# Performance work log

Hardware: AMD Instinct MI355X
Metric: run time of the kernel (lower is better)

## Reference

```python
import jax, jax.numpy as jnp
import numpy as np

B, L, DM, H, PD = 2, 1024, 512, 8, 64
D = DM // H  # head_dim = 64
NEG = -10000.0


def setup_inputs() -> dict:
    key = jax.random.key(0)
    ks = jax.random.split(key, 12)
    s = 1.0 / np.sqrt(DM)
    sp = 1.0 / np.sqrt(PD)
    return {
        "x": jax.random.normal(ks[0], (B, L, DM), dtype=jnp.float32),
        "z": jax.random.normal(ks[1], (B, L, L, PD), dtype=jnp.float32),
        "residue_mask": jnp.ones((B, L), dtype=bool),
        "Wq": jax.random.normal(ks[2], (DM, DM), dtype=jnp.float32) * s,
        "bq": jnp.zeros((DM,), dtype=jnp.float32),
        "Wk": jax.random.normal(ks[3], (DM, DM), dtype=jnp.float32) * s,
        "bk": jnp.zeros((DM,), dtype=jnp.float32),
        "Wv": jax.random.normal(ks[4], (DM, DM), dtype=jnp.float32) * s,
        "bv": jnp.zeros((DM,), dtype=jnp.float32),
        "Wo": jax.random.normal(ks[5], (DM, DM), dtype=jnp.float32) * s,
        "bo": jnp.zeros((DM,), dtype=jnp.float32),
        "Wpb": jax.random.normal(ks[6], (PD, H), dtype=jnp.float32) * sp,
    }


def reference(x, z, residue_mask, Wq, bq, Wk, bk, Wv, bv, Wo, bo, Wpb):
    b, l, c = x.shape
    scale = 1.0 / np.sqrt(D)
    # projections -> (B, H, L, D)
    q = (x @ Wq + bq).reshape(b, l, H, D).transpose(0, 2, 1, 3)
    k = (x @ Wk + bk).reshape(b, l, H, D).transpose(0, 2, 1, 3)
    v = (x @ Wv + bv).reshape(b, l, H, D).transpose(0, 2, 1, 3)
    # pair bias: (B, L, L, PD) @ (PD, H) -> (B, H, L, L)
    bias = jnp.einsum('bijp,ph->bhij', z, Wpb)
    logits = jnp.einsum('bhid,bhjd->bhij', q, k) * scale + bias
    key_ok = residue_mask[:, None, None, :]
    query_ok = residue_mask[:, None, :, None]
    logits = jnp.where(key_ok, logits, NEG)
    logits = jnp.where(query_ok, logits, NEG)
    attn = jax.nn.softmax(logits, axis=-1)
    out = jnp.einsum('bhij,bhjd->bhid', attn, v)
    out = out.transpose(0, 2, 1, 3).reshape(b, l, c)
    return out @ Wo + bo
```

## Files before the change

### kernel.cpp

```cpp
#include <hip/hip_runtime.h>

typedef __bf16 bf16;
typedef __attribute__((ext_vector_type(4))) __bf16 bf16x4;
typedef __attribute__((ext_vector_type(8))) __bf16 bf16x8;
typedef __attribute__((ext_vector_type(4))) float f32x4;
typedef __attribute__((ext_vector_type(4))) _Float16 f16x4;
typedef __attribute__((ext_vector_type(2))) _Float16 f16x2;

#define B_   2
#define L_   1024
#define DM_  512
#define H_   8
#define D_   64
#define PD_  64
#define NEG_VAL -10000.0f

#define XB_N   (2048*512)
#define WT_N   (1536*512)
#define WTO_N  (512*512)
#define WTPB_N (16*64)

static __device__ __forceinline__ f32x4 mfma_bf16(bf16x8 a, bf16x8 b, f32x4 c) {
  return __builtin_amdgcn_mfma_f32_16x16x32_bf16(a, b, c, 0, 0, 0);
}

__global__ __launch_bounds__(256) void prep_kernel(
    const float* __restrict__ x, const float* __restrict__ Wq, const float* __restrict__ Wk,
    const float* __restrict__ Wv, const float* __restrict__ Wo, const float* __restrict__ Wpb,
    bf16* __restrict__ xb, bf16* __restrict__ Wt, bf16* __restrict__ Wto, bf16* __restrict__ Wtpb) {
  const int total = XB_N + WT_N + WTO_N + WTPB_N;
  for (int idx = blockIdx.x * 256 + threadIdx.x; idx < total; idx += gridDim.x * 256) {
    if (idx < XB_N) {
      xb[idx] = (bf16)x[idx];
    } else if (idx < XB_N + WT_N) {
      int t = idx - XB_N;
      int n = t >> 9, kk = t & 511;
      int sel = n >> 9, nn = n & 511;
      const float* W = sel == 0 ? Wq : (sel == 1 ? Wk : Wv);
      Wt[t] = (bf16)W[kk * 512 + nn];
    } else if (idx < XB_N + WT_N + WTO_N) {
      int t = idx - XB_N - WT_N;
      int n = t >> 9, kk = t & 511;
      Wto[t] = (bf16)Wo[kk * 512 + n];
    } else {
      int t = idx - XB_N - WT_N - WTO_N;
      int n = t >> 6, kk = t & 63;
      Wtpb[t] = (n < 8) ? (bf16)Wpb[kk * 8 + n] : (bf16)0.0f;
    }
  }
}

__global__ __launch_bounds__(256) void qkv_gemm(
    const bf16* __restrict__ xb, const bf16* __restrict__ Wt,
    const float* __restrict__ bq, const float* __restrict__ bk, const float* __restrict__ bv,
    bf16* __restrict__ qb, bf16* __restrict__ kb, bf16* __restrict__ vT) {
  int wid = blockIdx.x * 4 + (threadIdx.x >> 6);
  int lane = threadIdx.x & 63;
  int mt = wid / 48, nt = wid - mt * 48;
  int row0 = mt * 32, col0 = nt * 32;
  int lr = lane & 15, lg = lane >> 4;
  const bf16* a0p = xb + (row0 + lr) * 512 + lg * 8;
  const bf16* a1p = a0p + 16 * 512;
  const bf16* b0p = Wt + (col0 + lr) * 512 + lg * 8;
  const bf16* b1p = b0p + 16 * 512;
  f32x4 acc00 = {0.f,0.f,0.f,0.f}, acc01 = acc00, acc10 = acc00, acc11 = acc00;
#pragma unroll
  for (int kk = 0; kk < 512; kk += 32) {
    bf16x8 a0 = *reinterpret_cast<const bf16x8*>(a0p + kk);
    bf16x8 a1 = *reinterpret_cast<const bf16x8*>(a1p + kk);
    bf16x8 b0 = *reinterpret_cast<const bf16x8*>(b0p + kk);
    bf16x8 b1 = *reinterpret_cast<const bf16x8*>(b1p + kk);
    acc00 = mfma_bf16(a0, b0, acc00);
    acc01 = mfma_bf16(a0, b1, acc01);
    acc10 = mfma_bf16(a1, b0, acc10);
    acc11 = mfma_bf16(a1, b1, acc11);
  }
#pragma unroll
  for (int ni = 0; ni < 2; ++ni) {
    int col = col0 + ni * 16 + lr;
    int wsel = col >> 9;
    int ncol = col & 511;
    int h = ncol >> 6, d = ncol & 63;
    const float* bias = wsel == 0 ? bq : (wsel == 1 ? bk : bv);
    float bval = bias[ncol];
#pragma unroll
    for (int mi = 0; mi < 2; ++mi) {
      f32x4 acc = (mi == 0) ? (ni == 0 ? acc00 : acc01) : (ni == 0 ? acc10 : acc11);
      int m0 = row0 + mi * 16 + lg * 4;
      int bidx = m0 >> 10, l0 = m0 & 1023;
      if (wsel == 2) {
        bf16x4 pv;
#pragma unroll
        for (int r = 0; r < 4; ++r) pv[r] = (bf16)(acc[r] + bval);
        *reinterpret_cast<bf16x4*>(vT + ((long)(bidx * H_ + h) * D_ + d) * L_ + l0) = pv;
      } else if (wsel == 0) {
#pragma unroll
        for (int r = 0; r < 4; ++r)
          qb[((long)(bidx * H_ + h) * L_ + l0 + r) * D_ + d] = (bf16)((acc[r] + bval) * 0.125f);
      } else {
#pragma unroll
        for (int r = 0; r < 4; ++r)
          kb[((long)(bidx * H_ + h) * L_ + l0 + r) * D_ + d] = (bf16)(acc[r] + bval);
      }
    }
  }
}

__global__ __launch_bounds__(256) void bias_gemm(
    const float* __restrict__ z, const bf16* __restrict__ Wtpb, _Float16* __restrict__ biasbuf) {
  __shared__ _Float16 bt[8][72];
  int w = threadIdx.x >> 6, lane = threadIdx.x & 63;
  int lr = lane & 15, lg = lane >> 4;
  long p0 = (long)blockIdx.x * 64 + w * 16;
  const float* zr = z + (p0 + lr) * 64;
  f32x4 z0 = *reinterpret_cast<const f32x4*>(zr + lg * 8);
  f32x4 z1 = *reinterpret_cast<const f32x4*>(zr + lg * 8 + 4);
  f32x4 z2 = *reinterpret_cast<const f32x4*>(zr + 32 + lg * 8);
  f32x4 z3 = *reinterpret_cast<const f32x4*>(zr + 32 + lg * 8 + 4);
  bf16x8 a0, a1;
#pragma unroll
  for (int e = 0; e < 4; ++e) { a0[e] = (bf16)z0[e]; a0[e + 4] = (bf16)z1[e]; }
#pragma unroll
  for (int e = 0; e < 4; ++e) { a1[e] = (bf16)z2[e]; a1[e + 4] = (bf16)z3[e]; }
  bf16x8 b0 = *reinterpret_cast<const bf16x8*>(Wtpb + lr * 64 + lg * 8);
  bf16x8 b1 = *reinterpret_cast<const bf16x8*>(Wtpb + lr * 64 + 32 + lg * 8);
  f32x4 acc = {0.f, 0.f, 0.f, 0.f};
  acc = mfma_bf16(a0, b0, acc);
  acc = mfma_bf16(a1, b1, acc);
  if (lr < 8) {
    f16x4 hv;
#pragma unroll
    for (int r = 0; r < 4; ++r) hv[r] = (_Float16)acc[r];
    *reinterpret_cast<f16x4*>(&bt[lr][w * 16 + lg * 4]) = hv;
  }
  __syncthreads();
  {
    int h = threadIdx.x >> 5, part = threadIdx.x & 31;
    long pb = (long)blockIdx.x * 64;
    int b = (int)(pb >> 20), i = ((int)(pb >> 10)) & 1023, j0 = (int)pb & 1023;
    _Float16* dst = biasbuf + ((((long)b * H_ + h) * L_ + i) << 10) + j0 + part * 2;
    *reinterpret_cast<f16x2*>(dst) = *reinterpret_cast<const f16x2*>(&bt[h][part * 2]);
  }
}

__global__ __launch_bounds__(256) void attn_kernel(
    const bf16* __restrict__ qb, const bf16* __restrict__ kb, const bf16* __restrict__ vT,
    const _Float16* __restrict__ biasbuf, const int* __restrict__ mask, bf16* __restrict__ attn_out) {
  __shared__ bf16  p_lds[4][16][64];
  __shared__ float o_lds[4][16][64];
  __shared__ float m_lds[4][16];
  __shared__ float l_lds[4][16];
  int bid = blockIdx.x;
  int b = bid >> 9, h = (bid >> 6) & 7, it = bid & 63;
  int i0 = it * 16;
  int tid = threadIdx.x, w = tid >> 6, lane = tid & 63, lr = lane & 15, lg = lane >> 4;

  const bf16* qrow = qb + ((long)(b * H_ + h) * L_ + i0 + lr) * D_ + lg * 8;
  bf16x8 qa0 = *reinterpret_cast<const bf16x8*>(qrow);
  bf16x8 qa1 = *reinterpret_cast<const bf16x8*>(qrow + 32);
  const bf16* kbase = kb + (long)(b * H_ + h) * L_ * D_;
  const bf16* vbase = vT + (long)(b * H_ + h) * D_ * L_;
  const _Float16* bias_base = biasbuf + ((long)(b * H_ + h) * L_ + i0) * L_;
  const int* mrow_mask = mask + b * L_;

  bool qok[4];
#pragma unroll
  for (int r = 0; r < 4; ++r) qok[r] = mrow_mask[i0 + lg * 4 + r] != 0;

  float mr[4] = {-3.0e38f, -3.0e38f, -3.0e38f, -3.0e38f};
  float lsum[4] = {0.f, 0.f, 0.f, 0.f};
  f32x4 o0 = {0.f,0.f,0.f,0.f}, o1 = o0, o2 = o0, o3 = o0;

  char* p_base = (char*)&p_lds[w][0][0];

  for (int jt = 0; jt < 4; ++jt) {
    int j0 = w * 256 + jt * 64;
    f32x4 s0, s1, s2, s3;
#pragma unroll
    for (int jsub = 0; jsub < 4; ++jsub) {
      int j = j0 + jsub * 16 + lr;
      f32x4 acc;
#pragma unroll
      for (int r = 0; r < 4; ++r) acc[r] = (float)bias_base[(long)(lg * 4 + r) * L_ + j];
      const bf16* kr = kbase + (long)j * D_ + lg * 8;
      acc = mfma_bf16(qa0, *reinterpret_cast<const bf16x8*>(kr), acc);
      acc = mfma_bf16(qa1, *reinterpret_cast<const bf16x8*>(kr + 32), acc);
      bool kok = mrow_mask[j] != 0;
      if (!kok) {
#pragma unroll
        for (int r = 0; r < 4; ++r) acc[r] = NEG_VAL;
      }
      if (jsub == 0) s0 = acc; else if (jsub == 1) s1 = acc; else if (jsub == 2) s2 = acc; else s3 = acc;
    }
#pragma unroll
    for (int r = 0; r < 4; ++r) {
      if (!qok[r]) { s0[r] = NEG_VAL; s1[r] = NEG_VAL; s2[r] = NEG_VAL; s3[r] = NEG_VAL; }
    }
#pragma unroll
    for (int r = 0; r < 4; ++r) {
      float mt_ = fmaxf(fmaxf(s0[r], s1[r]), fmaxf(s2[r], s3[r]));
#pragma unroll
      for (int off = 1; off <= 8; off <<= 1) mt_ = fmaxf(mt_, __shfl_xor(mt_, off));
      float mnew = fmaxf(mr[r], mt_);
      float alpha = __expf(mr[r] - mnew);
      mr[r] = mnew;
      float p0 = __expf(s0[r] - mnew);
      float p1 = __expf(s1[r] - mnew);
      float p2 = __expf(s2[r] - mnew);
      float p3 = __expf(s3[r] - mnew);
      float ps = p0 + p1 + p2 + p3;
#pragma unroll
      for (int off = 1; off <= 8; off <<= 1) ps += __shfl_xor(ps, off);
      lsum[r] = lsum[r] * alpha + ps;
      o0[r] *= alpha; o1[r] *= alpha; o2[r] *= alpha; o3[r] *= alpha;
      int row = lg * 4 + r;
      int sw = (row & 7) << 4;
      *(bf16*)(p_base + row * 128 + ((lr * 2) ^ sw)) = (bf16)p0;
      *(bf16*)(p_base + row * 128 + ((32 + lr * 2) ^ sw)) = (bf16)p1;
      *(bf16*)(p_base + row * 128 + ((64 + lr * 2) ^ sw)) = (bf16)p2;
      *(bf16*)(p_base + row * 128 + ((96 + lr * 2) ^ sw)) = (bf16)p3;
    }
    int swr = (lr & 7) << 4;
    bf16x8 pa0 = *(const bf16x8*)(p_base + lr * 128 + ((lg * 16) ^ swr));
    bf16x8 pa1 = *(const bf16x8*)(p_base + lr * 128 + ((64 + lg * 16) ^ swr));
#pragma unroll
    for (int dsub = 0; dsub < 4; ++dsub) {
      const bf16* vr = vbase + (long)(dsub * 16 + lr) * L_ + j0 + lg * 8;
      bf16x8 vb0 = *reinterpret_cast<const bf16x8*>(vr);
      bf16x8 vb1 = *reinterpret_cast<const bf16x8*>(vr + 32);
      f32x4 acc = (dsub == 0) ? o0 : (dsub == 1) ? o1 : (dsub == 2) ? o2 : o3;
      acc = mfma_bf16(pa0, vb0, acc);
      acc = mfma_bf16(pa1, vb1, acc);
      if (dsub == 0) o0 = acc; else if (dsub == 1) o1 = acc; else if (dsub == 2) o2 = acc; else o3 = acc;
    }
  }
#pragma unroll
  for (int r = 0; r < 4; ++r) {
    int row = lg * 4 + r;
    o_lds[w][row][0 * 16 + lr] = o0[r];
    o_lds[w][row][1 * 16 + lr] = o1[r];
    o_lds[w][row][2 * 16 + lr] = o2[r];
    o_lds[w][row][3 * 16 + lr] = o3[r];
    if (lr == 0) { m_lds[w][row] = mr[r]; l_lds[w][row] = lsum[r]; }
  }
  __syncthreads();
  {
    int row = tid >> 4, d0 = (tid & 15) * 4;
    float M = fmaxf(fmaxf(m_lds[0][row], m_lds[1][row]), fmaxf(m_lds[2][row], m_lds[3][row]));
    float lt = 0.f;
    float oacc[4] = {0.f, 0.f, 0.f, 0.f};
#pragma unroll
    for (int ww = 0; ww < 4; ++ww) {
      float c = __expf(m_lds[ww][row] - M);
      lt += c * l_lds[ww][row];
#pragma unroll
      for (int e = 0; e < 4; ++e) oacc[e] += c * o_lds[ww][row][d0 + e];
    }
    float inv = 1.0f / lt;
    bf16x4 ov;
#pragma unroll
    for (int e = 0; e < 4; ++e) ov[e] = (bf16)(oacc[e] * inv);
    *reinterpret_cast<bf16x4*>(attn_out + ((long)(b * L_ + i0 + row)) * DM_ + h * D_ + d0) = ov;
  }
}

__global__ __launch_bounds__(256) void out_gemm(
    const bf16* __restrict__ ab, const bf16* __restrict__ Wto,
    const float* __restrict__ bo, float* __restrict__ out) {
  int wid = blockIdx.x * 4 + (threadIdx.x >> 6);
  int lane = threadIdx.x & 63;
  int mt = wid >> 4, nt = wid & 15;
  int row0 = mt * 32, col0 = nt * 32;
  int lr = lane & 15, lg = lane >> 4;
  const bf16* a0p = ab + (row0 + lr) * 512 + lg * 8;
  const bf16* a1p = a0p + 16 * 512;
  const bf16* b0p = Wto + (col0 + lr) * 512 + lg * 8;
  const bf16* b1p = b0p + 16 * 512;
  f32x4 acc00 = {0.f,0.f,0.f,0.f}, acc01 = acc00, acc10 = acc00, acc11 = acc00;
#pragma unroll
  for (int kk = 0; kk < 512; kk += 32) {
    bf16x8 a0 = *reinterpret_cast<const bf16x8*>(a0p + kk);
    bf16x8 a1 = *reinterpret_cast<const bf16x8*>(a1p + kk);
    bf16x8 b0 = *reinterpret_cast<const bf16x8*>(b0p + kk);
    bf16x8 b1 = *reinterpret_cast<const bf16x8*>(b1p + kk);
    acc00 = mfma_bf16(a0, b0, acc00);
    acc01 = mfma_bf16(a0, b1, acc01);
    acc10 = mfma_bf16(a1, b0, acc10);
    acc11 = mfma_bf16(a1, b1, acc11);
  }
#pragma unroll
  for (int ni = 0; ni < 2; ++ni) {
    int col = col0 + ni * 16 + lr;
    float bval = bo[col];
#pragma unroll
    for (int mi = 0; mi < 2; ++mi) {
      f32x4 acc = (mi == 0) ? (ni == 0 ? acc00 : acc01) : (ni == 0 ? acc10 : acc11);
      int m0 = row0 + mi * 16 + lg * 4;
#pragma unroll
      for (int r = 0; r < 4; ++r) out[(long)(m0 + r) * 512 + col] = acc[r] + bval;
    }
  }
}

extern "C" void kernel_launch(void* const* d_in, const int* in_sizes, int n_in,
                              void* d_out, int out_size, void* d_ws, size_t ws_size,
                              hipStream_t stream) {
  const float* x    = (const float*)d_in[0];
  const float* z    = (const float*)d_in[1];
  const int*   mask = (const int*)d_in[2];
  const float* Wq   = (const float*)d_in[3];
  const float* bq   = (const float*)d_in[4];
  const float* Wk   = (const float*)d_in[5];
  const float* bk   = (const float*)d_in[6];
  const float* Wv   = (const float*)d_in[7];
  const float* bv   = (const float*)d_in[8];
  const float* Wo   = (const float*)d_in[9];
  const float* bo   = (const float*)d_in[10];
  const float* Wpb  = (const float*)d_in[11];

  char* ws = (char*)d_ws;
  bf16* xb        = (bf16*)(ws + 0);
  bf16* Wt        = (bf16*)(ws + 2097152);
  bf16* Wto       = (bf16*)(ws + 3670016);
  bf16* Wtpb      = (bf16*)(ws + 4194304);
  bf16* qbuf      = (bf16*)(ws + 4196352);
  bf16* kbuf      = (bf16*)(ws + 6293504);
  bf16* vTbuf     = (bf16*)(ws + 8390656);
  bf16* attn_out  = (bf16*)(ws + 10487808);
  _Float16* biasb = (_Float16*)(ws + 12584960);

  prep_kernel<<<2048, 256, 0, stream>>>(x, Wq, Wk, Wv, Wo, Wpb, xb, Wt, Wto, Wtpb);
  qkv_gemm<<<768, 256, 0, stream>>>(xb, Wt, bq, bk, bv, qbuf, kbuf, vTbuf);
  bias_gemm<<<32768, 256, 0, stream>>>(z, Wtpb, biasb);
  attn_kernel<<<1024, 256, 0, stream>>>(qbuf, kbuf, vTbuf, biasb, mask, attn_out);
  out_gemm<<<256, 256, 0, stream>>>(attn_out, Wto, bo, (float*)d_out);
}
```

Before: 191.1 us.

## Merge QKV and pair-bias GEMMs into one launch, tile-transpose weight prep

After: 205.1 us. 1.07x slower.

```diff
diff --git a/kernel.cpp b/kernel.cpp
--- a/kernel.cpp
+++ b/kernel.cpp
@@ -16,8 +16,6 @@
 #define NEG_VAL -10000.0f
 
 #define XB_N   (2048*512)
-#define WT_N   (1536*512)
-#define WTO_N  (512*512)
 #define WTPB_N (16*64)
 
 static __device__ __forceinline__ f32x4 mfma_bf16(bf16x8 a, bf16x8 b, f32x4 c) {
@@ -28,118 +26,143 @@
     const float* __restrict__ x, const float* __restrict__ Wq, const float* __restrict__ Wk,
     const float* __restrict__ Wv, const float* __restrict__ Wo, const float* __restrict__ Wpb,
     bf16* __restrict__ xb, bf16* __restrict__ Wt, bf16* __restrict__ Wto, bf16* __restrict__ Wtpb) {
-  const int total = XB_N + WT_N + WTO_N + WTPB_N;
-  for (int idx = blockIdx.x * 256 + threadIdx.x; idx < total; idx += gridDim.x * 256) {
-    if (idx < XB_N) {
-      xb[idx] = (bf16)x[idx];
-    } else if (idx < XB_N + WT_N) {
-      int t = idx - XB_N;
-      int n = t >> 9, kk = t & 511;
-      int sel = n >> 9, nn = n & 511;
-      const float* W = sel == 0 ? Wq : (sel == 1 ? Wk : Wv);
-      Wt[t] = (bf16)W[kk * 512 + nn];
-    } else if (idx < XB_N + WT_N + WTO_N) {
-      int t = idx - XB_N - WT_N;
-      int n = t >> 9, kk = t & 511;
-      Wto[t] = (bf16)Wo[kk * 512 + n];
+  __shared__ float td[32][33];
+  int bid = blockIdx.x, tid = threadIdx.x;
+  if (bid < 1024) {
+    int r = tid >> 3, c4 = (tid & 7) * 4;
+    const float* src;
+    bf16* dstbase;
+    int n0, k0, srcol;
+    if (bid < 768) {
+      int nt2 = bid >> 4, kt = bid & 15;
+      n0 = nt2 * 32; k0 = kt * 32;
+      int sel = n0 >> 9;
+      src = sel == 0 ? Wq : (sel == 1 ? Wk : Wv);
+      srcol = n0 & 511;
+      dstbase = Wt + (long)n0 * 512;
     } else {
-      int t = idx - XB_N - WT_N - WTO_N;
+      int t2 = bid - 768;
+      int nt2 = t2 >> 4, kt = t2 & 15;
+      n0 = nt2 * 32; k0 = kt * 32;
+      src = Wo; srcol = n0;
+      dstbase = Wto + (long)n0 * 512;
+    }
+    f32x4 v = *reinterpret_cast<const f32x4*>(src + (long)(k0 + r) * 512 + srcol + c4);
+#pragma unroll
+    for (int e = 0; e < 4; ++e) td[r][c4 + e] = v[e];
+    __syncthreads();
+    int nl = tid >> 3, k4 = (tid & 7) * 4;
+    bf16x4 o;
+#pragma unroll
+    for (int e = 0; e < 4; ++e) o[e] = (bf16)td[k4 + e][nl];
+    *reinterpret_cast<bf16x4*>(dstbase + (long)nl * 512 + k0 + k4) = o;
+  } else if (bid < 2048) {
+    int base = (bid - 1024) * 1024 + tid * 4;
+    f32x4 v = *reinterpret_cast<const f32x4*>(x + base);
+    bf16x4 o;
+#pragma unroll
+    for (int e = 0; e < 4; ++e) o[e] = (bf16)v[e];
+    *reinterpret_cast<bf16x4*>(xb + base) = o;
+  } else {
+    for (int t = tid; t < WTPB_N; t += 256) {
       int n = t >> 6, kk = t & 63;
       Wtpb[t] = (n < 8) ? (bf16)Wpb[kk * 8 + n] : (bf16)0.0f;
     }
   }
 }
 
-__global__ __launch_bounds__(256) void qkv_gemm(
+__global__ __launch_bounds__(256) void qkv_bias(
     const bf16* __restrict__ xb, const bf16* __restrict__ Wt,
     const float* __restrict__ bq, const float* __restrict__ bk, const float* __restrict__ bv,
-    bf16* __restrict__ qb, bf16* __restrict__ kb, bf16* __restrict__ vT) {
-  int wid = blockIdx.x * 4 + (threadIdx.x >> 6);
-  int lane = threadIdx.x & 63;
-  int mt = wid / 48, nt = wid - mt * 48;
-  int row0 = mt * 32, col0 = nt * 32;
-  int lr = lane & 15, lg = lane >> 4;
-  const bf16* a0p = xb + (row0 + lr) * 512 + lg * 8;
-  const bf16* a1p = a0p + 16 * 512;
-  const bf16* b0p = Wt + (col0 + lr) * 512 + lg * 8;
-  const bf16* b1p = b0p + 16 * 512;
-  f32x4 acc00 = {0.f,0.f,0.f,0.f}, acc01 = acc00, acc10 = acc00, acc11 = acc00;
-#pragma unroll
-  for (int kk = 0; kk < 512; kk += 32) {
-    bf16x8 a0 = *reinterpret_cast<const bf16x8*>(a0p + kk);
-    bf16x8 a1 = *reinterpret_cast<const bf16x8*>(a1p + kk);
-    bf16x8 b0 = *reinterpret_cast<const bf16x8*>(b0p + kk);
-    bf16x8 b1 = *reinterpret_cast<const bf16x8*>(b1p + kk);
-    acc00 = mfma_bf16(a0, b0, acc00);
-    acc01 = mfma_bf16(a0, b1, acc01);
-    acc10 = mfma_bf16(a1, b0, acc10);
-    acc11 = mfma_bf16(a1, b1, acc11);
-  }
-#pragma unroll
-  for (int ni = 0; ni < 2; ++ni) {
-    int col = col0 + ni * 16 + lr;
-    int wsel = col >> 9;
-    int ncol = col & 511;
-    int h = ncol >> 6, d = ncol & 63;
-    const float* bias = wsel == 0 ? bq : (wsel == 1 ? bk : bv);
-    float bval = bias[ncol];
-#pragma unroll
-    for (int mi = 0; mi < 2; ++mi) {
-      f32x4 acc = (mi == 0) ? (ni == 0 ? acc00 : acc01) : (ni == 0 ? acc10 : acc11);
-      int m0 = row0 + mi * 16 + lg * 4;
-      int bidx = m0 >> 10, l0 = m0 & 1023;
-      if (wsel == 2) {
-        bf16x4 pv;
-#pragma unroll
-        for (int r = 0; r < 4; ++r) pv[r] = (bf16)(acc[r] + bval);
-        *reinterpret_cast<bf16x4*>(vT + ((long)(bidx * H_ + h) * D_ + d) * L_ + l0) = pv;
-      } else if (wsel == 0) {
-#pragma unroll
-        for (int r = 0; r < 4; ++r)
-          qb[((long)(bidx * H_ + h) * L_ + l0 + r) * D_ + d] = (bf16)((acc[r] + bval) * 0.125f);
-      } else {
-#pragma unroll
-        for (int r = 0; r < 4; ++r)
-          kb[((long)(bidx * H_ + h) * L_ + l0 + r) * D_ + d] = (bf16)(acc[r] + bval);
+    bf16* __restrict__ qb, bf16* __restrict__ kb, bf16* __restrict__ vT,
+    const float* __restrict__ z, const bf16* __restrict__ Wtpb, _Float16* __restrict__ biasbuf) {
+  __shared__ _Float16 bt[2][8][72];
+  if (blockIdx.x < 768) {
+    int wid = blockIdx.x * 4 + (threadIdx.x >> 6);
+    int lane = threadIdx.x & 63;
+    int mt = wid / 48, nt = wid - mt * 48;
+    int row0 = mt * 32, col0 = nt * 32;
+    int lr = lane & 15, lg = lane >> 4;
+    const bf16* a0p = xb + (row0 + lr) * 512 + lg * 8;
+    const bf16* a1p = a0p + 16 * 512;
+    const bf16* b0p = Wt + (col0 + lr) * 512 + lg * 8;
+    const bf16* b1p = b0p + 16 * 512;
+    f32x4 acc00 = {0.f,0.f,0.f,0.f}, acc01 = acc00, acc10 = acc00, acc11 = acc00;
+#pragma unroll
+    for (int kk = 0; kk < 512; kk += 32) {
+      bf16x8 a0 = *reinterpret_cast<const bf16x8*>(a0p + kk);
+      bf16x8 a1 = *reinterpret_cast<const bf16x8*>(a1p + kk);
+      bf16x8 b0 = *reinterpret_cast<const bf16x8*>(b0p + kk);
+      bf16x8 b1 = *reinterpret_cast<const bf16x8*>(b1p + kk);
+      acc00 = mfma_bf16(a0, b0, acc00);
+      acc01 = mfma_bf16(a0, b1, acc01);
+      acc10 = mfma_bf16(a1, b0, acc10);
+      acc11 = mfma_bf16(a1, b1, acc11);
+    }
+#pragma unroll
+    for (int ni = 0; ni < 2; ++ni) {
+      int col = col0 + ni * 16 + lr;
+      int wsel = col >> 9;
+      int ncol = col & 511;
+      int h = ncol >> 6, d = ncol & 63;
+      const float* bias = wsel == 0 ? bq : (wsel == 1 ? bk : bv);
+      float bval = bias[ncol];
+#pragma unroll
+      for (int mi = 0; mi < 2; ++mi) {
+        f32x4 acc = (mi == 0) ? (ni == 0 ? acc00 : acc01) : (ni == 0 ? acc10 : acc11);
+        int m0 = row0 + mi * 16 + lg * 4;
+        int bidx = m0 >> 10, l0 = m0 & 1023;
+        if (wsel == 2) {
+          bf16x4 pv;
+#pragma unroll
+          for (int r = 0; r < 4; ++r) pv[r] = (bf16)(acc[r] + bval);
+          *reinterpret_cast<bf16x4*>(vT + ((long)(bidx * H_ + h) * D_ + d) * L_ + l0) = pv;
+        } else if (wsel == 0) {
+#pragma unroll
+          for (int r = 0; r < 4; ++r)
+            qb[((long)(bidx * H_ + h) * L_ + l0 + r) * D_ + d] = (bf16)((acc[r] + bval) * 0.125f);
+        } else {
+#pragma unroll
+          for (int r = 0; r < 4; ++r)
+            kb[((long)(bidx * H_ + h) * L_ + l0 + r) * D_ + d] = (bf16)(acc[r] + bval);
+        }
       }
     }
-  }
-}
-
-__global__ __launch_bounds__(256) void bias_gemm(
-    const float* __restrict__ z, const bf16* __restrict__ Wtpb, _Float16* __restrict__ biasbuf) {
-  __shared__ _Float16 bt[8][72];
-  int w = threadIdx.x >> 6, lane = threadIdx.x & 63;
-  int lr = lane & 15, lg = lane >> 4;
-  long p0 = (long)blockIdx.x * 64 + w * 16;
-  const float* zr = z + (p0 + lr) * 64;
-  f32x4 z0 = *reinterpret_cast<const f32x4*>(zr + lg * 8);
-  f32x4 z1 = *reinterpret_cast<const f32x4*>(zr + lg * 8 + 4);
-  f32x4 z2 = *reinterpret_cast<const f32x4*>(zr + 32 + lg * 8);
-  f32x4 z3 = *reinterpret_cast<const f32x4*>(zr + 32 + lg * 8 + 4);
-  bf16x8 a0, a1;
-#pragma unroll
-  for (int e = 0; e < 4; ++e) { a0[e] = (bf16)z0[e]; a0[e + 4] = (bf16)z1[e]; }
-#pragma unroll
-  for (int e = 0; e < 4; ++e) { a1[e] = (bf16)z2[e]; a1[e + 4] = (bf16)z3[e]; }
-  bf16x8 b0 = *reinterpret_cast<const bf16x8*>(Wtpb + lr * 64 + lg * 8);
-  bf16x8 b1 = *reinterpret_cast<const bf16x8*>(Wtpb + lr * 64 + 32 + lg * 8);
-  f32x4 acc = {0.f, 0.f, 0.f, 0.f};
-  acc = mfma_bf16(a0, b0, acc);
-  acc = mfma_bf16(a1, b1, acc);
-  if (lr < 8) {
-    f16x4 hv;
-#pragma unroll
-    for (int r = 0; r < 4; ++r) hv[r] = (_Float16)acc[r];
-    *reinterpret_cast<f16x4*>(&bt[lr][w * 16 + lg * 4]) = hv;
-  }
-  __syncthreads();
-  {
-    int h = threadIdx.x >> 5, part = threadIdx.x & 31;
-    long pb = (long)blockIdx.x * 64;
-    int b = (int)(pb >> 20), i = ((int)(pb >> 10)) & 1023, j0 = (int)pb & 1023;
-    _Float16* dst = biasbuf + ((((long)b * H_ + h) * L_ + i) << 10) + j0 + part * 2;
-    *reinterpret_cast<f16x2*>(dst) = *reinterpret_cast<const f16x2*>(&bt[h][part * 2]);
+  } else {
+    int bb = blockIdx.x - 768;
+    int w = threadIdx.x >> 6, lane = threadIdx.x & 63;
+    int lr = lane & 15, lg = lane >> 4;
+    bf16x8 wb0 = *reinterpret_cast<const bf16x8*>(Wtpb + lr * 64 + lg * 8);
+    bf16x8 wb1 = *reinterpret_cast<const bf16x8*>(Wtpb + lr * 64 + 32 + lg * 8);
+    int hh = threadIdx.x >> 5, part = threadIdx.x & 31;
+#pragma unroll
+    for (int g = 0; g < 4; ++g) {
+      long p0 = (long)bb * 256 + g * 64 + w * 16;
+      const float* zr = z + (p0 + lr) * 64;
+      f32x4 z0 = __builtin_nontemporal_load(reinterpret_cast<const f32x4*>(zr + lg * 8));
+      f32x4 z1 = __builtin_nontemporal_load(reinterpret_cast<const f32x4*>(zr + lg * 8 + 4));
+      f32x4 z2 = __builtin_nontemporal_load(reinterpret_cast<const f32x4*>(zr + 32 + lg * 8));
+      f32x4 z3 = __builtin_nontemporal_load(reinterpret_cast<const f32x4*>(zr + 32 + lg * 8 + 4));
+      bf16x8 a0, a1;
+#pragma unroll
+      for (int e = 0; e < 4; ++e) { a0[e] = (bf16)z0[e]; a0[e + 4] = (bf16)z1[e]; }
+#pragma unroll
+      for (int e = 0; e < 4; ++e) { a1[e] = (bf16)z2[e]; a1[e + 4] = (bf16)z3[e]; }
+      f32x4 acc = {0.f, 0.f, 0.f, 0.f};
+      acc = mfma_bf16(a0, wb0, acc);
+      acc = mfma_bf16(a1, wb1, acc);
+      if (lr < 8) {
+        f16x4 hv;
+#pragma unroll
+        for (int r = 0; r < 4; ++r) hv[r] = (_Float16)acc[r];
+        *reinterpret_cast<f16x4*>(&bt[g & 1][lr][w * 16 + lg * 4]) = hv;
+      }
+      __syncthreads();
+      long pb = (long)bb * 256 + g * 64;
+      int b_ = (int)(pb >> 20), i = ((int)(pb >> 10)) & 1023, j0 = (int)pb & 1023;
+      _Float16* dst = biasbuf + ((((long)b_ * H_ + hh) * L_ + i) << 10) + j0 + part * 2;
+      *reinterpret_cast<f16x2*>(dst) = *reinterpret_cast<const f16x2*>(&bt[g & 1][hh][part * 2]);
+    }
   }
 }
 
@@ -329,9 +352,9 @@
   bf16* attn_out  = (bf16*)(ws + 10487808);
   _Float16* biasb = (_Float16*)(ws + 12584960);
 
-  prep_kernel<<<2048, 256, 0, stream>>>(x, Wq, Wk, Wv, Wo, Wpb, xb, Wt, Wto, Wtpb);
-  qkv_gemm<<<768, 256, 0, stream>>>(xb, Wt, bq, bk, bv, qbuf, kbuf, vTbuf);
-  bias_gemm<<<32768, 256, 0, stream>>>(z, Wtpb, biasb);
+  prep_kernel<<<2049, 256, 0, stream>>>(x, Wq, Wk, Wv, Wo, Wpb, xb, Wt, Wto, Wtpb);
+  qkv_bias<<<768 + 8192, 256, 0, stream>>>(xb, Wt, bq, bk, bv, qbuf, kbuf, vTbuf,
+                                           z, Wtpb, biasb);
   attn_kernel<<<1024, 256, 0, stream>>>(qbuf, kbuf, vTbuf, biasb, mask, attn_out);
   out_gemm<<<256, 256, 0, stream>>>(attn_out, Wto, bo, (float*)d_out);
 }
```
